# Kernel optimization log

Hardware: AMD Instinct MI355X
Metric: run time of the kernel (lower is better)

Reference implementation:

```python
import jax, jax.numpy as jnp
import numpy as np

B, T = 64, 4096
ATTN_RNN_DIM, HYPERNET_DIM = 1024, 256
CHANNELS, KERNEL_SIZE, OUT_DIM = 32, 31, 128
PAD = (KERNEL_SIZE - 1) // 2


def setup_inputs() -> dict:
    key = jax.random.key(0)
    ks = jax.random.split(key, 8)
    s = 0.02
    return {
        "query": jax.random.normal(ks[0], (B, ATTN_RNN_DIM), jnp.float32),
        "prev_attn": jax.random.uniform(ks[1], (B, T), jnp.float32),
        "W1": jax.random.normal(ks[2], (HYPERNET_DIM, ATTN_RNN_DIM), jnp.float32) * s,
        "b1": jnp.zeros((HYPERNET_DIM,), jnp.float32),
        "W2": jax.random.normal(ks[3], (CHANNELS * KERNEL_SIZE, HYPERNET_DIM), jnp.float32) * s,
        "b2": jnp.zeros((CHANNELS * KERNEL_SIZE,), jnp.float32),
        "Wfc": jax.random.normal(ks[4], (OUT_DIM, CHANNELS), jnp.float32) * s,
        "bfc": jnp.zeros((OUT_DIM,), jnp.float32),
    }


def reference(query, prev_attn, W1, b1, W2, b2, Wfc, bfc):
    # hypernet: Linear -> tanh -> Linear, producing per-sample conv weights
    h = jnp.tanh(query @ W1.T + b1)                       # [B, hypernet_dim]
    convweight = (h @ W2.T + b2).reshape(B, CHANNELS, KERNEL_SIZE)  # [B, C, K]

    # per-sample depthwise conv1d (cross-correlation, 'same' padding)
    padded = jnp.pad(prev_attn, ((0, 0), (PAD, PAD)))     # [B, T+K-1]
    idx = jnp.arange(KERNEL_SIZE)[:, None] + jnp.arange(T)[None, :]  # [K, T]
    windows = padded[:, idx]                              # [B, K, T]
    x = jnp.einsum('bck,bkt->btc', convweight, windows)   # [B, T, C]

    # output linear
    return x @ Wfc.T + bfc                                # [B, T, out_dim]
```

## Files before the change

kernel.cpp:

```cpp
#include <hip/hip_runtime.h>

#define B 64
#define T 4096
#define AD 1024
#define HD 256
#define CH 32
#define KS 31
#define OD 128
#define PADW 15
#define CWN (CH*KS)
#define TILE_T 128
#define NTILE (T / TILE_T)

__global__ __launch_bounds__(256) void k_hyper1(const float* __restrict__ q,
        const float* __restrict__ W1, const float* __restrict__ b1,
        float* __restrict__ h) {
    int wid  = blockIdx.x * 4 + (threadIdx.x >> 6);
    int lane = threadIdx.x & 63;
    int b = wid >> 8;
    int j = wid & 255;
    const float4* qr = (const float4*)(q  + (size_t)b * AD);
    const float4* wr = (const float4*)(W1 + (size_t)j * AD);
    float s = 0.f;
    #pragma unroll
    for (int m = 0; m < 4; ++m) {
        float4 a = qr[m * 64 + lane];
        float4 w = wr[m * 64 + lane];
        s += a.x * w.x + a.y * w.y + a.z * w.z + a.w * w.w;
    }
    #pragma unroll
    for (int off = 32; off > 0; off >>= 1)
        s += __shfl_down(s, off, 64);
    if (lane == 0) h[b * HD + j] = tanhf(s + b1[j]);
}

__global__ __launch_bounds__(256) void k_cwG(const float* __restrict__ h,
        const float* __restrict__ W2, const float* __restrict__ b2,
        const float* __restrict__ Wfc, float* __restrict__ Gt) {
    int b = blockIdx.x >> 2;
    int q = blockIdx.x & 3;
    int tid = threadIdx.x;
    __shared__ float hs[HD];
    __shared__ float cwl[CH * 8];
    __shared__ float wfs_t[CH * OD];
    hs[tid] = h[(size_t)b * HD + tid];
    #pragma unroll
    for (int p = 0; p < 16; ++p) {
        int idx = p * 256 + tid;
        int o = idx >> 5, c = idx & 31;
        wfs_t[c * OD + o] = Wfc[idx];
    }
    __syncthreads();
    {
        int c = tid >> 3, kk = tid & 7;
        int k = q * 8 + kk;
        if (k < KS) {
            int r = c * KS + k;
            const float4* wr  = (const float4*)(W2 + (size_t)r * HD);
            const float4* hs4 = (const float4*)hs;
            float s = 0.f;
            #pragma unroll
            for (int m = 0; m < HD / 4; ++m) {
                float4 w = wr[m], hv = hs4[m];
                s += w.x * hv.x + w.y * hv.y + w.z * hv.z + w.w * hv.w;
            }
            cwl[c * 8 + kk] = s + b2[r];
        }
    }
    __syncthreads();
    #pragma unroll
    for (int p = 0; p < 4; ++p) {
        int idx = p * 256 + tid;
        int kl = idx >> 7, o = idx & 127;
        int kg = q * 8 + kl;
        if (kg < KS) {
            float s = 0.f;
            #pragma unroll
            for (int c = 0; c < CH; ++c)
                s += wfs_t[c * OD + o] * cwl[c * 8 + kl];
            Gt[(size_t)b * (KS * OD) + kg * OD + o] = s;
        }
    }
}

__device__ __forceinline__ void compute_chunk(const float* pa, int s0, float base,
                                              const float (&g)[KS], float (&acc)[8]) {
    float pw[40];
    const float4* lp = (const float4*)(pa + s0);
    #pragma unroll
    for (int q4 = 0; q4 < 10; ++q4) {
        float4 v = lp[q4];
        pw[q4*4+0] = v.x; pw[q4*4+1] = v.y; pw[q4*4+2] = v.z; pw[q4*4+3] = v.w;
    }
    #pragma unroll
    for (int tt = 0; tt < 8; ++tt) {
        float a = base;
        #pragma unroll
        for (int k = 0; k < KS; ++k)
            a += g[k] * pw[tt + k];
        acc[tt] = a;
    }
}

__global__ __launch_bounds__(256, 4) void k_conv(const float* __restrict__ pa_g,
        const float* __restrict__ Gt, const float* __restrict__ bfc,
        float* __restrict__ out) {
    int bid  = blockIdx.x;
    int sid  = (bid & 7) * 256 + (bid >> 3);
    int b    = sid >> 5;
    int tile = sid & 31;
    int t0   = tile * TILE_T;
    int tid  = threadIdx.x;
    __shared__ float tileo[64][128];
    __shared__ float pa[TILE_T + 32];

    if (tid < TILE_T + 30) {
        int gg = t0 + tid - PADW;
        pa[tid] = (gg >= 0 && gg < T) ? pa_g[(size_t)b * T + gg] : 0.f;
    }
    int o = tid & 127, half = tid >> 7;
    float g[KS];
    #pragma unroll
    for (int k = 0; k < KS; ++k)
        g[k] = Gt[(size_t)b * (KS * OD) + k * OD + o];
    float base = bfc[o];
    __syncthreads();

    #pragma unroll
    for (int pass = 0; pass < 2; ++pass) {
        const float* pap = pa + pass * 64;
        size_t obase = ((size_t)b * T + t0 + pass * 64) * OD;
        #pragma unroll
        for (int c = 0; c < 4; ++c) {
            int s0 = half * 32 + c * 8;
            float acc[8];
            compute_chunk(pap, s0, base, g, acc);
            #pragma unroll
            for (int tt = 0; tt < 8; ++tt)
                tileo[s0 + tt][o] = acc[tt];
            __syncthreads();
            #pragma unroll
            for (int j = 0; j < 2; ++j) {
                int f  = j * 256 + tid;
                int rl = f >> 5, c4 = f & 31;
                int row = (j == 0) ? (c * 8 + rl) : (32 + c * 8 + (rl - 8));
                float4 v = *(const float4*)&tileo[row][c4 * 4];
                *(float4*)(out + obase + (size_t)row * OD + c4 * 4) = v;
            }
        }
    }
}

extern "C" void kernel_launch(void* const* d_in, const int* in_sizes, int n_in,
                              void* d_out, int out_size, void* d_ws, size_t ws_size,
                              hipStream_t stream) {
    const float* query = (const float*)d_in[0];
    const float* prev  = (const float*)d_in[1];
    const float* W1    = (const float*)d_in[2];
    const float* b1    = (const float*)d_in[3];
    const float* W2    = (const float*)d_in[4];
    const float* b2    = (const float*)d_in[5];
    const float* Wfc   = (const float*)d_in[6];
    const float* bfc   = (const float*)d_in[7];
    float* out = (float*)d_out;

    float* h  = (float*)d_ws;
    float* Gt = h + B * HD;

    k_hyper1<<<dim3(4096), dim3(256), 0, stream>>>(query, W1, b1, h);
    k_cwG   <<<dim3(B * 4), dim3(256), 0, stream>>>(h, W2, b2, Wfc, Gt);
    k_conv  <<<dim3(B * NTILE), dim3(256), 0, stream>>>(prev, Gt, bfc, out);
}
```

Measured before the change: 53.04 us.

## Drop LDS output staging in conv, compute two outputs per thread, split cwG wider

The conv kernel now has each thread produce two adjacent output channels for eight rows and write them directly as float2 to global memory. This removes the shared-memory transpose tile and the per-chunk barriers. The hypernet weight kernel is split into eight k-slices per batch, with a wave-cooperative dot product and XCD-aware block mapping, so it gets more parallelism. In exchange, conv stores become 8-byte instead of 16-byte and register pressure roughly doubles (the g array becomes float2), so the occupancy hint drops from 4 to 3 blocks per CU.

```diff
diff --git a/kernel.cpp b/kernel.cpp
--- a/kernel.cpp
+++ b/kernel.cpp
@@ -37,72 +37,60 @@
 __global__ __launch_bounds__(256) void k_cwG(const float* __restrict__ h,
         const float* __restrict__ W2, const float* __restrict__ b2,
         const float* __restrict__ Wfc, float* __restrict__ Gt) {
-    int b = blockIdx.x >> 2;
-    int q = blockIdx.x & 3;
+    int bid = blockIdx.x;
+    int xcd = bid & 7, idx = bid >> 3;
+    int b   = xcd * 8 + (idx >> 3);
+    int oct = idx & 7;
     int tid = threadIdx.x;
+    int lane = tid & 63, w = tid >> 6;
     __shared__ float hs[HD];
-    __shared__ float cwl[CH * 8];
+    __shared__ float cwl[CH * 4];
     __shared__ float wfs_t[CH * OD];
+
     hs[tid] = h[(size_t)b * HD + tid];
     #pragma unroll
     for (int p = 0; p < 16; ++p) {
-        int idx = p * 256 + tid;
-        int o = idx >> 5, c = idx & 31;
-        wfs_t[c * OD + o] = Wfc[idx];
+        int i2 = p * 256 + tid;
+        int o = i2 >> 5, c = i2 & 31;
+        wfs_t[c * OD + o] = Wfc[i2];
     }
     __syncthreads();
-    {
-        int c = tid >> 3, kk = tid & 7;
-        int k = q * 8 + kk;
-        if (k < KS) {
-            int r = c * KS + k;
-            const float4* wr  = (const float4*)(W2 + (size_t)r * HD);
-            const float4* hs4 = (const float4*)hs;
-            float s = 0.f;
+
+    const float4* hs4 = (const float4*)hs;
+    float4 hv = hs4[lane];
+    #pragma unroll
+    for (int i = 0; i < 32; ++i) {
+        int n = w * 32 + i;
+        int c = n >> 2, kl = n & 3;
+        int kg = oct * 4 + kl;
+        if (kg < KS) {
+            int r = c * KS + kg;
+            float4 wv = ((const float4*)(W2 + (size_t)r * HD))[lane];
+            float s = wv.x * hv.x + wv.y * hv.y + wv.z * hv.z + wv.w * hv.w;
             #pragma unroll
-            for (int m = 0; m < HD / 4; ++m) {
-                float4 w = wr[m], hv = hs4[m];
-                s += w.x * hv.x + w.y * hv.y + w.z * hv.z + w.w * hv.w;
-            }
-            cwl[c * 8 + kk] = s + b2[r];
+            for (int m = 32; m > 0; m >>= 1)
+                s += __shfl_xor(s, m, 64);
+            if (lane == 0) cwl[c * 4 + kl] = s + b2[r];
         }
     }
     __syncthreads();
+
     #pragma unroll
-    for (int p = 0; p < 4; ++p) {
-        int idx = p * 256 + tid;
-        int kl = idx >> 7, o = idx & 127;
-        int kg = q * 8 + kl;
+    for (int p = 0; p < 2; ++p) {
+        int i2 = p * 256 + tid;
+        int kl = i2 >> 7, o = i2 & 127;
+        int kg = oct * 4 + kl;
         if (kg < KS) {
             float s = 0.f;
             #pragma unroll
             for (int c = 0; c < CH; ++c)
-                s += wfs_t[c * OD + o] * cwl[c * 8 + kl];
+                s += wfs_t[c * OD + o] * cwl[c * 4 + kl];
             Gt[(size_t)b * (KS * OD) + kg * OD + o] = s;
         }
     }
 }
 
-__device__ __forceinline__ void compute_chunk(const float* pa, int s0, float base,
-                                              const float (&g)[KS], float (&acc)[8]) {
-    float pw[40];
-    const float4* lp = (const float4*)(pa + s0);
-    #pragma unroll
-    for (int q4 = 0; q4 < 10; ++q4) {
-        float4 v = lp[q4];
-        pw[q4*4+0] = v.x; pw[q4*4+1] = v.y; pw[q4*4+2] = v.z; pw[q4*4+3] = v.w;
-    }
-    #pragma unroll
-    for (int tt = 0; tt < 8; ++tt) {
-        float a = base;
-        #pragma unroll
-        for (int k = 0; k < KS; ++k)
-            a += g[k] * pw[tt + k];
-        acc[tt] = a;
-    }
-}
-
-__global__ __launch_bounds__(256, 4) void k_conv(const float* __restrict__ pa_g,
+__global__ __launch_bounds__(256, 3) void k_conv(const float* __restrict__ pa_g,
         const float* __restrict__ Gt, const float* __restrict__ bfc,
         float* __restrict__ out) {
     int bid  = blockIdx.x;
@@ -111,42 +99,43 @@
     int tile = sid & 31;
     int t0   = tile * TILE_T;
     int tid  = threadIdx.x;
-    __shared__ float tileo[64][128];
-    __shared__ float pa[TILE_T + 32];
+    int lane = tid & 63, w = tid >> 6;
+    __shared__ float pa[160];
 
     if (tid < TILE_T + 30) {
         int gg = t0 + tid - PADW;
         pa[tid] = (gg >= 0 && gg < T) ? pa_g[(size_t)b * T + gg] : 0.f;
     }
-    int o = tid & 127, half = tid >> 7;
-    float g[KS];
+    int o2 = lane * 2;
+    float2 g2[KS];
+    const float* gp = Gt + (size_t)b * (KS * OD) + o2;
     #pragma unroll
     for (int k = 0; k < KS; ++k)
-        g[k] = Gt[(size_t)b * (KS * OD) + k * OD + o];
-    float base = bfc[o];
+        g2[k] = *(const float2*)(gp + k * OD);
+    float2 bias = *(const float2*)(bfc + o2);
     __syncthreads();
 
+    float* outb = out + ((size_t)b * T + t0) * OD + o2;
     #pragma unroll
-    for (int pass = 0; pass < 2; ++pass) {
-        const float* pap = pa + pass * 64;
-        size_t obase = ((size_t)b * T + t0 + pass * 64) * OD;
+    for (int it = 0; it < 4; ++it) {
+        int r0 = it * 32 + w * 8;
+        float pw[40];
+        const float4* pv = (const float4*)(pa + r0);
         #pragma unroll
-        for (int c = 0; c < 4; ++c) {
-            int s0 = half * 32 + c * 8;
-            float acc[8];
-            compute_chunk(pap, s0, base, g, acc);
+        for (int q4 = 0; q4 < 10; ++q4) {
+            float4 v = pv[q4];
+            pw[q4*4+0] = v.x; pw[q4*4+1] = v.y; pw[q4*4+2] = v.z; pw[q4*4+3] = v.w;
+        }
+        #pragma unroll
+        for (int r = 0; r < 8; ++r) {
+            float2 a = bias;
             #pragma unroll
-            for (int tt = 0; tt < 8; ++tt)
-                tileo[s0 + tt][o] = acc[tt];
-            __syncthreads();
-            #pragma unroll
-            for (int j = 0; j < 2; ++j) {
-                int f  = j * 256 + tid;
-                int rl = f >> 5, c4 = f & 31;
-                int row = (j == 0) ? (c * 8 + rl) : (32 + c * 8 + (rl - 8));
-                float4 v = *(const float4*)&tileo[row][c4 * 4];
-                *(float4*)(out + obase + (size_t)row * OD + c4 * 4) = v;
+            for (int k = 0; k < KS; ++k) {
+                float p = pw[r + k];
+                a.x += g2[k].x * p;
+                a.y += g2[k].y * p;
             }
+            *(float2*)(outb + (size_t)(r0 + r) * OD) = a;
         }
     }
 }
@@ -168,6 +157,6 @@
     float* Gt = h + B * HD;
 
     k_hyper1<<<dim3(4096), dim3(256), 0, stream>>>(query, W1, b1, h);
-    k_cwG   <<<dim3(B * 4), dim3(256), 0, stream>>>(h, W2, b2, Wfc, Gt);
+    k_cwG   <<<dim3(B * 8), dim3(256), 0, stream>>>(h, W2, b2, Wfc, Gt);
     k_conv  <<<dim3(B * NTILE), dim3(256), 0, stream>>>(prev, Gt, bfc, out);
 }
```

Result: slower. 62.30 us (+17.5%).
